# Kernel tuning notes

Measured on AMD Instinct MI355X. Metric: run time of the kernel, lower is better.

## Reference

```python
import jax, jax.numpy as jnp
import numpy as np

B, C, DM, H = 2, 256, 512, 8
D = DM // H          # d_head = 64
SPARSE_K = 64


def setup_inputs() -> dict:
    key = jax.random.key(0)
    ks = jax.random.split(key, 12)
    s = 0.02
    return {
        "x": jax.random.normal(ks[0], (B, C, DM), dtype=jnp.float32),
        "Wq": jax.random.normal(ks[1], (DM, DM), dtype=jnp.float32) * s,
        "bq": jnp.zeros((DM,), jnp.float32),
        "Wk": jax.random.normal(ks[2], (DM, DM), dtype=jnp.float32) * s,
        "bk": jnp.zeros((DM,), jnp.float32),
        "Wv": jax.random.normal(ks[3], (DM, DM), dtype=jnp.float32) * s,
        "bv": jnp.zeros((DM,), jnp.float32),
        "w1": jax.random.normal(ks[4], (D, 3 * D), dtype=jnp.float32) * s,
        "b1": jax.random.normal(ks[5], (D,), dtype=jnp.float32) * s,
        "w2": jax.random.normal(ks[6], (1, D), dtype=jnp.float32) * s,
        "b2": jax.random.normal(ks[7], (1,), dtype=jnp.float32) * s,
        "Wo": jax.random.normal(ks[8], (DM, DM), dtype=jnp.float32) * s,
        "bo": jnp.zeros((DM,), jnp.float32),
    }


def _heads(x, W, b):
    # torch Linear: x @ W.T + b, then (B,C,H,d) -> (B,H,C,d)
    y = jnp.einsum("bcD,ED->bcE", x, W) + b
    return y.reshape(B, C, H, D).transpose(0, 2, 1, 3)


def reference(x, Wq, bq, Wk, bk, Wv, bv, w1, b1, w2, b2, Wo, bo):
    q = _heads(x, Wq, bq)  # (B,H,C,d)
    k = _heads(x, Wk, bk)
    v = _heads(x, Wv, bv)

    # split first MLP layer weight: [:, :d] acts on q, [:, d:2d] on k, [:, 2d:] on q*k
    q_p = jnp.einsum("bhcd,ed->bhce", q, w1[:, :D])
    k_p = jnp.einsum("bhcd,ed->bhce", k, w1[:, D:2 * D])

    # res: (B,H,C,C,d)
    res = q_p[:, :, :, None, :] + k_p[:, :, None, :, :] + b1
    interaction = q[:, :, :, None, :] * k[:, :, None, :, :]
    res = res + jnp.einsum("bhije,fe->bhijf", interaction, w1[:, 2 * D:])

    # second MLP layer -> scalar score per pair, exact (erf) GELU as torch default
    h = jax.nn.gelu(res, approximate=False)
    scores = (jnp.einsum("bhijd,od->bhijo", h, w2) + b2)[..., 0]
    scores = scores / jnp.sqrt(jnp.float32(D))

    if SPARSE_K < C:
        top_vals = jax.lax.top_k(scores, SPARSE_K)[0]
        thresh = top_vals[..., -1:]
        scores = jnp.where(scores >= thresh, scores, jnp.float32(-1e9))

    attn = jax.nn.softmax(scores, axis=-1)  # dropout is identity (p=0 / eval)
    out = jnp.einsum("bhij,bhjd->bhid", attn, v)
    out = out.transpose(0, 2, 1, 3).reshape(B, C, DM)
    return jnp.einsum("bcD,ED->bcE", out, Wo) + bo
```

## Files before the change

### kernel.cpp

```cpp
#include <hip/hip_runtime.h>
#include <math.h>

typedef _Float16 fp16;
typedef __attribute__((ext_vector_type(4))) _Float16 f16x4;
typedef __attribute__((ext_vector_type(8))) _Float16 f16x8;
typedef __attribute__((ext_vector_type(4))) float floatx4;
typedef __attribute__((ext_vector_type(2))) float f32x2;

__device__ __forceinline__ f32x2 mk2(float a, float b) { f32x2 r; r.x = a; r.y = b; return r; }
__device__ __forceinline__ f32x2 sp2(float a) { f32x2 r; r.x = a; r.y = a; return r; }

__device__ __forceinline__ f32x2 gelu2(f32x2 x) {
    f32x2 tt = x * 0.70710678118654752440f;
    f32x2 s  = tt * tt;
    f32x2 p  = __builtin_elementwise_fma(s, sp2(-8.548327023450852e-4f), sp2(5.223977625442188e-3f));
    p = __builtin_elementwise_fma(s, p, sp2(-2.6866170645131252e-2f));
    p = __builtin_elementwise_fma(s, p, sp2(0.11283791670955126f));
    p = __builtin_elementwise_fma(s, p, sp2(-0.3761263890318375f));
    p = __builtin_elementwise_fma(s, p, sp2(1.1283791670955126f));
    f32x2 e = tt * p;
    if (__builtin_expect(fabsf(tt.x) > 0.5f, 0)) e.x = erff(tt.x);
    if (__builtin_expect(fabsf(tt.y) > 0.5f, 0)) e.y = erff(tt.y);
    f32x2 hx = x * 0.5f;
    return __builtin_elementwise_fma(hx, e, hx);
}

__device__ __forceinline__ void split2(float a, fp16& h, fp16& m) {
    h = (fp16)a;
    m = (fp16)(a - (float)h);
}

struct SplitArgs {
    const float* src[5];
    fp16* h[5]; fp16* m[5];
};

__global__ __launch_bounds__(256) void split2_512_kernel(SplitArgs S) {
    int z = blockIdx.z;
    const float* src = S.src[z];
    fp16* dh = S.h[z]; fp16* dm = S.m[z];
    int t = blockIdx.x * 256 + threadIdx.x;
    int row = t >> 7, kq = (t & 127) * 4;
    int rt = row >> 4, rm = row & 15;
    int ks = kq >> 5, q4 = (kq >> 3) & 3, u0 = kq & 7;
    int dst = ((rt * 16 + ks) * 64 + q4 * 16 + rm) * 8 + u0;
    float4 vv = *(const float4*)&src[row * 512 + kq];
    float a4[4] = {vv.x, vv.y, vv.z, vv.w};
    f16x4 h, m;
    #pragma unroll
    for (int u = 0; u < 4; u++) {
        fp16 hh, mm;
        split2(a4[u], hh, mm);
        h[u] = hh; m[u] = mm;
    }
    *(f16x4*)&dh[dst] = h;
    *(f16x4*)&dm[dst] = m;
}

struct MM2Args {
    const fp16 *Ah, *Am;
    const fp16 *Wh[3], *Wm[3];
    const float* bias[3];
    float* outf[3];
    fp16 *kh, *km;
    int mode[3];
};

__global__ __launch_bounds__(64) void mm_mfma_kernel(MM2Args A) {
    const int z = blockIdx.z;
    const fp16* Wh = A.Wh[z]; const fp16* Wm = A.Wm[z];
    const float* bias = A.bias[z];
    const int lane = threadIdx.x;
    const int m16 = lane & 15, q4 = lane >> 4;
    const int mt = blockIdx.y, bx = blockIdx.x;

    floatx4 acc0, acc1;
    {
        float bv = bias[bx * 16 + m16];
        acc0[0] = bv; acc0[1] = bv; acc0[2] = bv; acc0[3] = bv;
        acc1[0] = 0.f; acc1[1] = 0.f; acc1[2] = 0.f; acc1[3] = 0.f;
    }

    #pragma unroll 4
    for (int ks = 0; ks < 16; ks++) {
        int sa = ((mt * 16 + ks) * 64 + lane) * 8;
        f16x8 ah = *(const f16x8*)&A.Ah[sa];
        f16x8 am = *(const f16x8*)&A.Am[sa];
        int sw = ((bx * 16 + ks) * 64 + lane) * 8;
        f16x8 wh = *(const f16x8*)&Wh[sw];
        f16x8 wm = *(const f16x8*)&Wm[sw];
        acc0 = __builtin_amdgcn_mfma_f32_16x16x32_f16(ah, wh, acc0, 0, 0, 0);
        acc1 = __builtin_amdgcn_mfma_f32_16x16x32_f16(ah, wm, acc1, 0, 0, 0);
        acc0 = __builtin_amdgcn_mfma_f32_16x16x32_f16(am, wh, acc0, 0, 0, 0);
        acc1 = __builtin_amdgcn_mfma_f32_16x16x32_f16(am, wm, acc1, 0, 0, 0);
    }
    floatx4 acc = acc0 + acc1;

    const int mode = A.mode[z];
    const int n = bx * 16 + m16;
    #pragma unroll
    for (int r = 0; r < 4; r++) {
        int m = mt * 16 + q4 * 4 + r;
        float val = acc[r];
        if (mode == 0) {
            A.outf[z][m * 512 + n] = val;
        } else if (mode == 1) {
            A.outf[z][(((m >> 8) * 8 + (n >> 6)) * 256 + (m & 255)) * 64 + (n & 63)] = val;
        } else {
            int krow = ((m >> 8) * 8 + (n >> 6)) * 256 + (m & 255);
            int d = n & 63;
            int dst = (((krow >> 4) * 2 + (d >> 5)) * 64 + ((d >> 3) & 3) * 16 + (krow & 15)) * 8 + (d & 7);
            fp16 h, mm;
            split2(val, h, mm);
            A.kh[dst] = h; A.km[dst] = mm;
        }
    }
}

__global__ __launch_bounds__(256, 4) void fused_mfma_attn_kernel(
    const float* __restrict__ q, const float* __restrict__ v,
    const fp16* __restrict__ khi, const fp16* __restrict__ kmid,
    const float* __restrict__ w1, const float* __restrict__ b1,
    const float* __restrict__ w2, const float* __restrict__ b2,
    fp16* __restrict__ oh, fp16* __restrict__ om)
{
    const int i4 = blockIdx.x;
    const int bh = blockIdx.y;
    const int t  = threadIdx.x;
    const int lane = t & 63, w = t >> 6;
    const int m16 = lane & 15, q4 = lane >> 4;

    __shared__ f32x2 part2[4][256];
    __shared__ f32x2 sc2[2][256];
    __shared__ float qpb_s[2][64];
    __shared__ f32x2 sbuf2[2][256];
    __shared__ f32x2 red_s[2][4][64];
    __shared__ f32x2 red2_s[2][4];
    __shared__ f32x2 thr_s2[2], smax_s2[2];

    const int f = w * 16 + m16;
    const float* w1row = w1 + f * 192;
    const float4 w2f = *(const float4*)&w2[w * 16 + q4 * 4];
    const float b2v = b2[0];
    const float* qbase = q + (bh * 256 + i4 * 4) * 64;

    f32x2 score0, score1;

    #pragma unroll 1
    for (int p = 0; p < 2; p++) {
        f16x8 Ah[2][2], Am[2][2];
        float qa0 = 0.f, qa1 = 0.f;
        #pragma unroll
        for (int ks = 0; ks < 2; ks++) {
            #pragma unroll
            for (int u = 0; u < 2; u++) {
                int e = ks * 32 + q4 * 8 + u * 4;
                float4 wa = *(const float4*)&w1row[e];
                float4 wb = *(const float4*)&w1row[64 + e];
                float4 wc = *(const float4*)&w1row[128 + e];
                #pragma unroll
                for (int i01 = 0; i01 < 2; i01++) {
                    float4 qv = *(const float4*)&qbase[(2 * p + i01) * 64 + e];
                    float dq = wa.x * qv.x + wa.y * qv.y + wa.z * qv.z + wa.w * qv.w;
                    if (i01 == 0) qa0 += dq; else qa1 += dq;
                    float av[4];
                    av[0] = fmaf(wc.x, qv.x, wb.x);
                    av[1] = fmaf(wc.y, qv.y, wb.y);
                    av[2] = fmaf(wc.z, qv.z, wb.z);
                    av[3] = fmaf(wc.w, qv.w, wb.w);
                    #pragma unroll
                    for (int uu = 0; uu < 4; uu++) {
                        fp16 h, m;
                        split2(av[uu], h, m);
                        Ah[i01][ks][u * 4 + uu] = h;
                        Am[i01][ks][u * 4 + uu] = m;
                    }
                }
            }
        }
        qa0 += __shfl_xor(qa0, 16);
        qa0 += __shfl_xor(qa0, 32);
        qa1 += __shfl_xor(qa1, 16);
        qa1 += __shfl_xor(qa1, 32);
        if (lane < 16) {
            qpb_s[0][w * 16 + lane] = qa0 + b1[w * 16 + lane];
            qpb_s[1][w * 16 + lane] = qa1 + b1[w * 16 + lane];
        }
        __syncthreads();

        floatx4 qpbr0 = *(const floatx4*)&qpb_s[0][w * 16 + q4 * 4];
        floatx4 qpbr1 = *(const floatx4*)&qpb_s[1][w * 16 + q4 * 4];

        #pragma unroll 1
        for (int jt = 0; jt < 16; jt++) {
            int base = ((bh * 16 + jt) * 2 * 64 + lane) * 8;
            f16x8 Kh0 = *(const f16x8*)&khi [base];
            f16x8 Km0 = *(const f16x8*)&kmid[base];
            f16x8 Kh1 = *(const f16x8*)&khi [base + 512];
            f16x8 Km1 = *(const f16x8*)&kmid[base + 512];
            floatx4 a0 = qpbr0, a1 = qpbr1;
            floatx4 b0, b1v_;
            b0[0] = 0.f; b0[1] = 0.f; b0[2] = 0.f; b0[3] = 0.f;
            b1v_ = b0;
            a0   = __builtin_amdgcn_mfma_f32_16x16x32_f16(Ah[0][0], Kh0, a0,   0, 0, 0);
            a1   = __builtin_amdgcn_mfma_f32_16x16x32_f16(Ah[1][0], Kh0, a1,   0, 0, 0);
            b0   = __builtin_amdgcn_mfma_f32_16x16x32_f16(Ah[0][0], Km0, b0,   0, 0, 0);
            b1v_ = __builtin_amdgcn_mfma_f32_16x16x32_f16(Ah[1][0], Km0, b1v_, 0, 0, 0);
            a0   = __builtin_amdgcn_mfma_f32_16x16x32_f16(Am[0][0], Kh0, a0,   0, 0, 0);
            a1   = __builtin_amdgcn_mfma_f32_16x16x32_f16(Am[1][0], Kh0, a1,   0, 0, 0);
            b0   = __builtin_amdgcn_mfma_f32_16x16x32_f16(Am[0][0], Km0, b0,   0, 0, 0);
            b1v_ = __builtin_amdgcn_mfma_f32_16x16x32_f16(Am[1][0], Km0, b1v_, 0, 0, 0);
            a0   = __builtin_amdgcn_mfma_f32_16x16x32_f16(Ah[0][1], Kh1, a0,   0, 0, 0);
            a1   = __builtin_amdgcn_mfma_f32_16x16x32_f16(Ah[1][1], Kh1, a1,   0, 0, 0);
            b0   = __builtin_amdgcn_mfma_f32_16x16x32_f16(Ah[0][1], Km1, b0,   0, 0, 0);
            b1v_ = __builtin_amdgcn_mfma_f32_16x16x32_f16(Ah[1][1], Km1, b1v_, 0, 0, 0);
            a0   = __builtin_amdgcn_mfma_f32_16x16x32_f16(Am[0][1], Kh1, a0,   0, 0, 0);
            a1   = __builtin_amdgcn_mfma_f32_16x16x32_f16(Am[1][1], Kh1, a1,   0, 0, 0);
            b0   = __builtin_amdgcn_mfma_f32_16x16x32_f16(Am[0][1], Km1, b0,   0, 0, 0);
            b1v_ = __builtin_amdgcn_mfma_f32_16x16x32_f16(Am[1][1], Km1, b1v_, 0, 0, 0);
            a0 = a0 + b0; a1 = a1 + b1v_;
            f32x2 g0 = gelu2(mk2(a0[0], a1[0]));
            f32x2 g1 = gelu2(mk2(a0[1], a1[1]));
            f32x2 g2 = gelu2(mk2(a0[2], a1[2]));
            f32x2 g3 = gelu2(mk2(a0[3], a1[3]));
            f32x2 sA = __builtin_elementwise_fma(g1, sp2(w2f.y), g0 * w2f.x);
            f32x2 sB = __builtin_elementwise_fma(g3, sp2(w2f.w), g2 * w2f.z);
            f32x2 s = sA + sB;
            s.x += __shfl_xor(s.x, 16);
            s.y += __shfl_xor(s.y, 16);
            s.x += __shfl_xor(s.x, 32);
            s.y += __shfl_xor(s.y, 32);
            if (lane < 16) part2[w][jt * 16 + lane] = s;
        }
        __syncthreads();

        f32x2 sc = ((part2[0][t] + part2[1][t]) +
                    (part2[2][t] + part2[3][t]) + b2v) * 0.125f;
        if (p == 0) score0 = sc; else score1 = sc;
    }

    f32x2 sv0 = score0, sv1 = score1;
    #pragma unroll
    for (int k = 2; k <= 256; k <<= 1) {
        #pragma unroll
        for (int j = k >> 1; j >= 1; j >>= 1) {
            f32x2 pv0, pv1;
            if (j >= 64) {
                sbuf2[0][t] = sv0; sbuf2[1][t] = sv1;
                __syncthreads();
                pv0 = sbuf2[0][t ^ j]; pv1 = sbuf2[1][t ^ j];
                __syncthreads();
            } else {
                pv0.x = __shfl_xor(sv0.x, j);
                pv0.y = __shfl_xor(sv0.y, j);
                pv1.x = __shfl_xor(sv1.x, j);
                pv1.y = __shfl_xor(sv1.y, j);
            }
            bool keepMin = (((t & j) == 0) == ((t & k) == 0));
            f32x2 mn0 = __builtin_elementwise_min(sv0, pv0);
            f32x2 mx0 = __builtin_elementwise_max(sv0, pv0);
            f32x2 mn1 = __builtin_elementwise_min(sv1, pv1);
            f32x2 mx1 = __builtin_elementwise_max(sv1, pv1);
            sv0 = keepMin ? mn0 : mx0;
            sv1 = keepMin ? mn1 : mx1;
        }
    }
    if (t == 192) { thr_s2[0]  = sv0; thr_s2[1]  = sv1; }
    if (t == 255) { smax_s2[0] = sv0; smax_s2[1] = sv1; }
    __syncthreads();

    float p00 = (score0.x >= thr_s2[0].x) ? __expf(score0.x - smax_s2[0].x) : 0.0f;
    float p01 = (score0.y >= thr_s2[0].y) ? __expf(score0.y - smax_s2[0].y) : 0.0f;
    float p10 = (score1.x >= thr_s2[1].x) ? __expf(score1.x - smax_s2[1].x) : 0.0f;
    float p11 = (score1.y >= thr_s2[1].y) ? __expf(score1.y - smax_s2[1].y) : 0.0f;
    sc2[0][t] = mk2(p00, p01);
    sc2[1][t] = mk2(p10, p11);
    f32x2 ps0 = mk2(p00, p01), ps1 = mk2(p10, p11);
    #pragma unroll
    for (int mask = 1; mask < 64; mask <<= 1) {
        ps0.x += __shfl_xor(ps0.x, mask);
        ps0.y += __shfl_xor(ps0.y, mask);
        ps1.x += __shfl_xor(ps1.x, mask);
        ps1.y += __shfl_xor(ps1.y, mask);
    }
    if (lane == 0) { red2_s[0][w] = ps0; red2_s[1][w] = ps1; }
    __syncthreads();
    f32x2 den0 = (red2_s[0][0] + red2_s[0][1]) + (red2_s[0][2] + red2_s[0][3]);
    f32x2 den1 = (red2_s[1][0] + red2_s[1][1]) + (red2_s[1][2] + red2_s[1][3]);
    f32x2 invp0 = mk2(1.0f / den0.x, 1.0f / den0.y);
    f32x2 invp1 = mk2(1.0f / den1.x, 1.0f / den1.y);

    const int d = t & 63, g = t >> 6;
    const float* vb = v + bh * 256 * 64;
    f32x2 av0 = mk2(0.f, 0.f), av1 = mk2(0.f, 0.f);
    f32x2 av0b = mk2(0.f, 0.f), av1b = mk2(0.f, 0.f);
    for (int j8 = 0; j8 < 8; j8++) {
        int jj = g * 64 + j8 * 8;
        float v0 = vb[(jj + 0) * 64 + d];
        float v1 = vb[(jj + 1) * 64 + d];
        float v2 = vb[(jj + 2) * 64 + d];
        float v3 = vb[(jj + 3) * 64 + d];
        float v4 = vb[(jj + 4) * 64 + d];
        float v5 = vb[(jj + 5) * 64 + d];
        float v6 = vb[(jj + 6) * 64 + d];
        float v7 = vb[(jj + 7) * 64 + d];
        av0  = __builtin_elementwise_fma(sc2[0][jj + 0], sp2(v0), av0);
        av1  = __builtin_elementwise_fma(sc2[1][jj + 0], sp2(v0), av1);
        av0b = __builtin_elementwise_fma(sc2[0][jj + 4], sp2(v4), av0b);
        av1b = __builtin_elementwise_fma(sc2[1][jj + 4], sp2(v4), av1b);
        av0  = __builtin_elementwise_fma(sc2[0][jj + 1], sp2(v1), av0);
        av1  = __builtin_elementwise_fma(sc2[1][jj + 1], sp2(v1), av1);
        av0b = __builtin_elementwise_fma(sc2[0][jj + 5], sp2(v5), av0b);
        av1b = __builtin_elementwise_fma(sc2[1][jj + 5], sp2(v5), av1b);
        av0  = __builtin_elementwise_fma(sc2[0][jj + 2], sp2(v2), av0);
        av1  = __builtin_elementwise_fma(sc2[1][jj + 2], sp2(v2), av1);
        av0b = __builtin_elementwise_fma(sc2[0][jj + 6], sp2(v6), av0b);
        av1b = __builtin_elementwise_fma(sc2[1][jj + 6], sp2(v6), av1b);
        av0  = __builtin_elementwise_fma(sc2[0][jj + 3], sp2(v3), av0);
        av1  = __builtin_elementwise_fma(sc2[1][jj + 3], sp2(v3), av1);
        av0b = __builtin_elementwise_fma(sc2[0][jj + 7], sp2(v7), av0b);
        av1b = __builtin_elementwise_fma(sc2[1][jj + 7], sp2(v7), av1b);
    }
    red_s[0][g][d] = av0 + av0b;
    red_s[1][g][d] = av1 + av1b;
    __syncthreads();

    {
        int i01 = t >> 6, dd = t & 63;
        int pr = i01 >> 1, comp = i01 & 1;
        f32x2 osum = (red_s[pr][0][dd] + red_s[pr][1][dd]) +
                     (red_s[pr][2][dd] + red_s[pr][3][dd]);
        f32x2 iv = pr ? invp1 : invp0;
        float o = (comp ? osum.y : osum.x) * (comp ? iv.y : iv.x);
        int b = bh >> 3, h = bh & 7;
        int row = b * 256 + i4 * 4 + i01;
        int n = h * 64 + dd;
        int dst = (((row >> 4) * 16 + (n >> 5)) * 64 + ((n >> 3) & 3) * 16 + (row & 15)) * 8 + (n & 7);
        fp16 hh, mm;
        split2(o, hh, mm);
        oh[dst] = hh; om[dst] = mm;
    }
}

extern "C" void kernel_launch(void* const* d_in, const int* in_sizes, int n_in,
                              void* d_out, int out_size, void* d_ws, size_t ws_size,
                              hipStream_t stream) {
    const float* x  = (const float*)d_in[0];
    const float* Wq = (const float*)d_in[1];
    const float* bq = (const float*)d_in[2];
    const float* Wk = (const float*)d_in[3];
    const float* bk = (const float*)d_in[4];
    const float* Wv = (const float*)d_in[5];
    const float* bv = (const float*)d_in[6];
    const float* w1 = (const float*)d_in[7];
    const float* b1 = (const float*)d_in[8];
    const float* w2 = (const float*)d_in[9];
    const float* b2 = (const float*)d_in[10];
    const float* Wo = (const float*)d_in[11];
    const float* bo = (const float*)d_in[12];
    float* out = (float*)d_out;

    const int NE = 262144;
    float* qb  = (float*)d_ws;
    float* vb  = qb + NE;
    fp16* base = (fp16*)(vb + NE);
    fp16* khi  = base;            fp16* kmid = khi + NE;
    fp16* xs   = kmid + NE;
    fp16* wqs  = xs  + 2 * NE;
    fp16* wks  = wqs + 2 * NE;
    fp16* wvs  = wks + 2 * NE;
    fp16* wos  = wvs + 2 * NE;
    fp16* oas  = wos + 2 * NE;

    {
        SplitArgs S;
        const float* srcs[5] = {x, Wq, Wk, Wv, Wo};
        fp16* dsts[5] = {xs, wqs, wks, wvs, wos};
        for (int z = 0; z < 5; z++) {
            S.src[z] = srcs[z];
            S.h[z] = dsts[z]; S.m[z] = dsts[z] + NE;
        }
        split2_512_kernel<<<dim3(256, 1, 5), 256, 0, stream>>>(S);
    }
    {
        MM2Args M;
        M.Ah = xs; M.Am = xs + NE;
        M.Wh[0] = wqs; M.Wm[0] = wqs + NE;
        M.Wh[1] = wks; M.Wm[1] = wks + NE;
        M.Wh[2] = wvs; M.Wm[2] = wvs + NE;
        M.bias[0] = bq; M.bias[1] = bk; M.bias[2] = bv;
        M.outf[0] = qb; M.outf[1] = nullptr; M.outf[2] = vb;
        M.kh = khi; M.km = kmid;
        M.mode[0] = 1; M.mode[1] = 2; M.mode[2] = 1;
        mm_mfma_kernel<<<dim3(32, 32, 3), 64, 0, stream>>>(M);
    }
    fused_mfma_attn_kernel<<<dim3(64, 16), 256, 0, stream>>>(
        qb, vb, khi, kmid, w1, b1, w2, b2,
        oas, oas + NE);
    {
        MM2Args M;
        M.Ah = oas; M.Am = oas + NE;
        M.Wh[0] = wos; M.Wm[0] = wos + NE;
        M.Wh[1] = wos; M.Wm[1] = wos;
        M.Wh[2] = wos; M.Wm[2] = wos;
        M.bias[0] = bo; M.bias[1] = bo; M.bias[2] = bo;
        M.outf[0] = out; M.outf[1] = out; M.outf[2] = out;
        M.kh = khi; M.km = kmid;
        M.mode[0] = 0; M.mode[1] = 0; M.mode[2] = 0;
        mm_mfma_kernel<<<dim3(32, 32, 1), 64, 0, stream>>>(M);
    }
}
```

Measured before the change: 164.6 us.

## Split fused score/top-k kernel into separate score and top-k attention kernels

Separates the pairwise MLP score computation from the top-k/softmax/AV stage, with the score kernel handling two query rows per block so it launches twice as many blocks. Scores are written to a global buffer carved from the no-longer-needed x split workspace and reloaded by the second kernel. This aims to raise occupancy and parallelism for the MFMA-heavy scoring phase, at the cost of an extra launch and a 4 MB global round trip for the scores.

Result: slower. 169.1 us (+2.7%).

```diff
diff --git a/kernel.cpp b/kernel.cpp
--- a/kernel.cpp
+++ b/kernel.cpp
@@ -117,127 +117,138 @@
     }
 }
 
-__global__ __launch_bounds__(256, 4) void fused_mfma_attn_kernel(
-    const float* __restrict__ q, const float* __restrict__ v,
+__global__ __launch_bounds__(256, 4) void score_kernel(
+    const float* __restrict__ q,
     const fp16* __restrict__ khi, const fp16* __restrict__ kmid,
     const float* __restrict__ w1, const float* __restrict__ b1,
     const float* __restrict__ w2, const float* __restrict__ b2,
+    float* __restrict__ scores)
+{
+    const int i2 = blockIdx.x;
+    const int bh = blockIdx.y;
+    const int t  = threadIdx.x;
+    const int lane = t & 63, w = t >> 6;
+    const int m16 = lane & 15, q4 = lane >> 4;
+
+    __shared__ f32x2 part2[4][256];
+    __shared__ float qpb_s[2][64];
+
+    const int f = w * 16 + m16;
+    const float* w1row = w1 + f * 192;
+    const float4 w2f = *(const float4*)&w2[w * 16 + q4 * 4];
+    const float b2v = b2[0];
+    const float* qbase = q + (bh * 256 + i2 * 2) * 64;
+
+    f16x8 Ah[2][2], Am[2][2];
+    float qa0 = 0.f, qa1 = 0.f;
+    #pragma unroll
+    for (int ks = 0; ks < 2; ks++) {
+        #pragma unroll
+        for (int u = 0; u < 2; u++) {
+            int e = ks * 32 + q4 * 8 + u * 4;
+            float4 wa = *(const float4*)&w1row[e];
+            float4 wb = *(const float4*)&w1row[64 + e];
+            float4 wc = *(const float4*)&w1row[128 + e];
+            #pragma unroll
+            for (int i01 = 0; i01 < 2; i01++) {
+                float4 qv = *(const float4*)&qbase[i01 * 64 + e];
+                float dq = wa.x * qv.x + wa.y * qv.y + wa.z * qv.z + wa.w * qv.w;
+                if (i01 == 0) qa0 += dq; else qa1 += dq;
+                float av[4];
+                av[0] = fmaf(wc.x, qv.x, wb.x);
+                av[1] = fmaf(wc.y, qv.y, wb.y);
+                av[2] = fmaf(wc.z, qv.z, wb.z);
+                av[3] = fmaf(wc.w, qv.w, wb.w);
+                #pragma unroll
+                for (int uu = 0; uu < 4; uu++) {
+                    fp16 h, m;
+                    split2(av[uu], h, m);
+                    Ah[i01][ks][u * 4 + uu] = h;
+                    Am[i01][ks][u * 4 + uu] = m;
+                }
+            }
+        }
+    }
+    qa0 += __shfl_xor(qa0, 16);
+    qa0 += __shfl_xor(qa0, 32);
+    qa1 += __shfl_xor(qa1, 16);
+    qa1 += __shfl_xor(qa1, 32);
+    if (lane < 16) {
+        qpb_s[0][w * 16 + lane] = qa0 + b1[w * 16 + lane];
+        qpb_s[1][w * 16 + lane] = qa1 + b1[w * 16 + lane];
+    }
+    __syncthreads();
+
+    floatx4 qpbr0 = *(const floatx4*)&qpb_s[0][w * 16 + q4 * 4];
+    floatx4 qpbr1 = *(const floatx4*)&qpb_s[1][w * 16 + q4 * 4];
+
+    #pragma unroll 1
+    for (int jt = 0; jt < 16; jt++) {
+        int base = ((bh * 16 + jt) * 2 * 64 + lane) * 8;
+        f16x8 Kh0 = *(const f16x8*)&khi [base];
+        f16x8 Km0 = *(const f16x8*)&kmid[base];
+        f16x8 Kh1 = *(const f16x8*)&khi [base + 512];
+        f16x8 Km1 = *(const f16x8*)&kmid[base + 512];
+        floatx4 a0 = qpbr0, a1 = qpbr1;
+        floatx4 b0, b1v_;
+        b0[0] = 0.f; b0[1] = 0.f; b0[2] = 0.f; b0[3] = 0.f;
+        b1v_ = b0;
+        a0   = __builtin_amdgcn_mfma_f32_16x16x32_f16(Ah[0][0], Kh0, a0,   0, 0, 0);
+        a1   = __builtin_amdgcn_mfma_f32_16x16x32_f16(Ah[1][0], Kh0, a1,   0, 0, 0);
+        b0   = __builtin_amdgcn_mfma_f32_16x16x32_f16(Ah[0][0], Km0, b0,   0, 0, 0);
+        b1v_ = __builtin_amdgcn_mfma_f32_16x16x32_f16(Ah[1][0], Km0, b1v_, 0, 0, 0);
+        a0   = __builtin_amdgcn_mfma_f32_16x16x32_f16(Am[0][0], Kh0, a0,   0, 0, 0);
+        a1   = __builtin_amdgcn_mfma_f32_16x16x32_f16(Am[1][0], Kh0, a1,   0, 0, 0);
+        b0   = __builtin_amdgcn_mfma_f32_16x16x32_f16(Am[0][0], Km0, b0,   0, 0, 0);
+        b1v_ = __builtin_amdgcn_mfma_f32_16x16x32_f16(Am[1][0], Km0, b1v_, 0, 0, 0);
+        a0   = __builtin_amdgcn_mfma_f32_16x16x32_f16(Ah[0][1], Kh1, a0,   0, 0, 0);
+        a1   = __builtin_amdgcn_mfma_f32_16x16x32_f16(Ah[1][1], Kh1, a1,   0, 0, 0);
+        b0   = __builtin_amdgcn_mfma_f32_16x16x32_f16(Ah[0][1], Km1, b0,   0, 0, 0);
+        b1v_ = __builtin_amdgcn_mfma_f32_16x16x32_f16(Ah[1][1], Km1, b1v_, 0, 0, 0);
+        a0   = __builtin_amdgcn_mfma_f32_16x16x32_f16(Am[0][1], Kh1, a0,   0, 0, 0);
+        a1   = __builtin_amdgcn_mfma_f32_16x16x32_f16(Am[1][1], Kh1, a1,   0, 0, 0);
+        b0   = __builtin_amdgcn_mfma_f32_16x16x32_f16(Am[0][1], Km1, b0,   0, 0, 0);
+        b1v_ = __builtin_amdgcn_mfma_f32_16x16x32_f16(Am[1][1], Km1, b1v_, 0, 0, 0);
+        a0 = a0 + b0; a1 = a1 + b1v_;
+        f32x2 g0 = gelu2(mk2(a0[0], a1[0]));
+        f32x2 g1 = gelu2(mk2(a0[1], a1[1]));
+        f32x2 g2 = gelu2(mk2(a0[2], a1[2]));
+        f32x2 g3 = gelu2(mk2(a0[3], a1[3]));
+        f32x2 sA = __builtin_elementwise_fma(g1, sp2(w2f.y), g0 * w2f.x);
+        f32x2 sB = __builtin_elementwise_fma(g3, sp2(w2f.w), g2 * w2f.z);
+        f32x2 s = sA + sB;
+        s.x += __shfl_xor(s.x, 16);
+        s.y += __shfl_xor(s.y, 16);
+        s.x += __shfl_xor(s.x, 32);
+        s.y += __shfl_xor(s.y, 32);
+        if (lane < 16) part2[w][jt * 16 + lane] = s;
+    }
+    __syncthreads();
+
+    f32x2 sc = ((part2[0][t] + part2[1][t]) +
+                (part2[2][t] + part2[3][t]) + b2v) * 0.125f;
+    scores[(bh * 256 + i2 * 2 + 0) * 256 + t] = sc.x;
+    scores[(bh * 256 + i2 * 2 + 1) * 256 + t] = sc.y;
+}
+
+__global__ __launch_bounds__(256, 4) void topk_attn_kernel(
+    const float* __restrict__ scores, const float* __restrict__ v,
     fp16* __restrict__ oh, fp16* __restrict__ om)
 {
     const int i4 = blockIdx.x;
     const int bh = blockIdx.y;
     const int t  = threadIdx.x;
     const int lane = t & 63, w = t >> 6;
-    const int m16 = lane & 15, q4 = lane >> 4;
-
-    __shared__ f32x2 part2[4][256];
+
     __shared__ f32x2 sc2[2][256];
-    __shared__ float qpb_s[2][64];
     __shared__ f32x2 sbuf2[2][256];
     __shared__ f32x2 red_s[2][4][64];
     __shared__ f32x2 red2_s[2][4];
     __shared__ f32x2 thr_s2[2], smax_s2[2];
 
-    const int f = w * 16 + m16;
-    const float* w1row = w1 + f * 192;
-    const float4 w2f = *(const float4*)&w2[w * 16 + q4 * 4];
-    const float b2v = b2[0];
-    const float* qbase = q + (bh * 256 + i4 * 4) * 64;
-
-    f32x2 score0, score1;
-
-    #pragma unroll 1
-    for (int p = 0; p < 2; p++) {
-        f16x8 Ah[2][2], Am[2][2];
-        float qa0 = 0.f, qa1 = 0.f;
-        #pragma unroll
-        for (int ks = 0; ks < 2; ks++) {
-            #pragma unroll
-            for (int u = 0; u < 2; u++) {
-                int e = ks * 32 + q4 * 8 + u * 4;
-                float4 wa = *(const float4*)&w1row[e];
-                float4 wb = *(const float4*)&w1row[64 + e];
-                float4 wc = *(const float4*)&w1row[128 + e];
-                #pragma unroll
-                for (int i01 = 0; i01 < 2; i01++) {
-                    float4 qv = *(const float4*)&qbase[(2 * p + i01) * 64 + e];
-                    float dq = wa.x * qv.x + wa.y * qv.y + wa.z * qv.z + wa.w * qv.w;
-                    if (i01 == 0) qa0 += dq; else qa1 += dq;
-                    float av[4];
-                    av[0] = fmaf(wc.x, qv.x, wb.x);
-                    av[1] = fmaf(wc.y, qv.y, wb.y);
-                    av[2] = fmaf(wc.z, qv.z, wb.z);
-                    av[3] = fmaf(wc.w, qv.w, wb.w);
-                    #pragma unroll
-                    for (int uu = 0; uu < 4; uu++) {
-                        fp16 h, m;
-                        split2(av[uu], h, m);
-                        Ah[i01][ks][u * 4 + uu] = h;
-                        Am[i01][ks][u * 4 + uu] = m;
-                    }
-                }
-            }
-        }
-        qa0 += __shfl_xor(qa0, 16);
-        qa0 += __shfl_xor(qa0, 32);
-        qa1 += __shfl_xor(qa1, 16);
-        qa1 += __shfl_xor(qa1, 32);
-        if (lane < 16) {
-            qpb_s[0][w * 16 + lane] = qa0 + b1[w * 16 + lane];
-            qpb_s[1][w * 16 + lane] = qa1 + b1[w * 16 + lane];
-        }
-        __syncthreads();
-
-        floatx4 qpbr0 = *(const floatx4*)&qpb_s[0][w * 16 + q4 * 4];
-        floatx4 qpbr1 = *(const floatx4*)&qpb_s[1][w * 16 + q4 * 4];
-
-        #pragma unroll 1
-        for (int jt = 0; jt < 16; jt++) {
-            int base = ((bh * 16 + jt) * 2 * 64 + lane) * 8;
-            f16x8 Kh0 = *(const f16x8*)&khi [base];
-            f16x8 Km0 = *(const f16x8*)&kmid[base];
-            f16x8 Kh1 = *(const f16x8*)&khi [base + 512];
-            f16x8 Km1 = *(const f16x8*)&kmid[base + 512];
-            floatx4 a0 = qpbr0, a1 = qpbr1;
-            floatx4 b0, b1v_;
-            b0[0] = 0.f; b0[1] = 0.f; b0[2] = 0.f; b0[3] = 0.f;
-            b1v_ = b0;
-            a0   = __builtin_amdgcn_mfma_f32_16x16x32_f16(Ah[0][0], Kh0, a0,   0, 0, 0);
-            a1   = __builtin_amdgcn_mfma_f32_16x16x32_f16(Ah[1][0], Kh0, a1,   0, 0, 0);
-            b0   = __builtin_amdgcn_mfma_f32_16x16x32_f16(Ah[0][0], Km0, b0,   0, 0, 0);
-            b1v_ = __builtin_amdgcn_mfma_f32_16x16x32_f16(Ah[1][0], Km0, b1v_, 0, 0, 0);
-            a0   = __builtin_amdgcn_mfma_f32_16x16x32_f16(Am[0][0], Kh0, a0,   0, 0, 0);
-            a1   = __builtin_amdgcn_mfma_f32_16x16x32_f16(Am[1][0], Kh0, a1,   0, 0, 0);
-            b0   = __builtin_amdgcn_mfma_f32_16x16x32_f16(Am[0][0], Km0, b0,   0, 0, 0);
-            b1v_ = __builtin_amdgcn_mfma_f32_16x16x32_f16(Am[1][0], Km0, b1v_, 0, 0, 0);
-            a0   = __builtin_amdgcn_mfma_f32_16x16x32_f16(Ah[0][1], Kh1, a0,   0, 0, 0);
-            a1   = __builtin_amdgcn_mfma_f32_16x16x32_f16(Ah[1][1], Kh1, a1,   0, 0, 0);
-            b0   = __builtin_amdgcn_mfma_f32_16x16x32_f16(Ah[0][1], Km1, b0,   0, 0, 0);
-            b1v_ = __builtin_amdgcn_mfma_f32_16x16x32_f16(Ah[1][1], Km1, b1v_, 0, 0, 0);
-            a0   = __builtin_amdgcn_mfma_f32_16x16x32_f16(Am[0][1], Kh1, a0,   0, 0, 0);
-            a1   = __builtin_amdgcn_mfma_f32_16x16x32_f16(Am[1][1], Kh1, a1,   0, 0, 0);
-            b0   = __builtin_amdgcn_mfma_f32_16x16x32_f16(Am[0][1], Km1, b0,   0, 0, 0);
-            b1v_ = __builtin_amdgcn_mfma_f32_16x16x32_f16(Am[1][1], Km1, b1v_, 0, 0, 0);
-            a0 = a0 + b0; a1 = a1 + b1v_;
-            f32x2 g0 = gelu2(mk2(a0[0], a1[0]));
-            f32x2 g1 = gelu2(mk2(a0[1], a1[1]));
-            f32x2 g2 = gelu2(mk2(a0[2], a1[2]));
-            f32x2 g3 = gelu2(mk2(a0[3], a1[3]));
-            f32x2 sA = __builtin_elementwise_fma(g1, sp2(w2f.y), g0 * w2f.x);
-            f32x2 sB = __builtin_elementwise_fma(g3, sp2(w2f.w), g2 * w2f.z);
-            f32x2 s = sA + sB;
-            s.x += __shfl_xor(s.x, 16);
-            s.y += __shfl_xor(s.y, 16);
-            s.x += __shfl_xor(s.x, 32);
-            s.y += __shfl_xor(s.y, 32);
-            if (lane < 16) part2[w][jt * 16 + lane] = s;
-        }
-        __syncthreads();
-
-        f32x2 sc = ((part2[0][t] + part2[1][t]) +
-                    (part2[2][t] + part2[3][t]) + b2v) * 0.125f;
-        if (p == 0) score0 = sc; else score1 = sc;
-    }
+    const float* sb = scores + (bh * 256 + i4 * 4) * 256;
+    f32x2 score0 = mk2(sb[t], sb[256 + t]);
+    f32x2 score1 = mk2(sb[512 + t], sb[768 + t]);
 
     f32x2 sv0 = score0, sv1 = score1;
     #pragma unroll
@@ -371,6 +382,7 @@
     fp16* wvs  = wks + 2 * NE;
     fp16* wos  = wvs + 2 * NE;
     fp16* oas  = wos + 2 * NE;
+    float* scores = (float*)xs;
 
     {
         SplitArgs S;
@@ -394,9 +406,10 @@
         M.mode[0] = 1; M.mode[1] = 2; M.mode[2] = 1;
         mm_mfma_kernel<<<dim3(32, 32, 3), 64, 0, stream>>>(M);
     }
-    fused_mfma_attn_kernel<<<dim3(64, 16), 256, 0, stream>>>(
-        qb, vb, khi, kmid, w1, b1, w2, b2,
-        oas, oas + NE);
+    score_kernel<<<dim3(128, 16), 256, 0, stream>>>(
+        qb, khi, kmid, w1, b1, w2, b2, scores);
+    topk_attn_kernel<<<dim3(64, 16), 256, 0, stream>>>(
+        scores, vb, oas, oas + NE);
     {
         MM2Args M;
         M.Ah = oas; M.Am = oas + NE;
```
